# Kernel tuning notes

Measured on AMD Instinct MI355X. Metric: run time of the kernel, lower is better.

Reference implementation:

```python
import jax, jax.numpy as jnp
import numpy as np

HIDDEN = 1024
HEADS = 16
D_K = HIDDEN // HEADS
NEG_INF = -jnp.inf


def setup_inputs() -> dict:
    key = jax.random.key(0)
    ks = jax.random.split(key, 9)
    N, S = 4, 2048
    scale = 1.0 / np.sqrt(HIDDEN)
    x = jax.random.normal(ks[0], (N, S, HIDDEN), dtype=jnp.float32)
    attn_mask = jnp.ones((N, S), dtype=jnp.int32)
    Wq = jax.random.normal(ks[1], (HIDDEN, HIDDEN), dtype=jnp.float32) * scale
    bq = jnp.zeros((HIDDEN,), dtype=jnp.float32)
    Wk = jax.random.normal(ks[2], (HIDDEN, HIDDEN), dtype=jnp.float32) * scale
    bk = jnp.zeros((HIDDEN,), dtype=jnp.float32)
    Wv = jax.random.normal(ks[3], (HIDDEN, HIDDEN), dtype=jnp.float32) * scale
    bv = jnp.zeros((HIDDEN,), dtype=jnp.float32)
    Wp = jax.random.normal(ks[4], (HIDDEN, HIDDEN), dtype=jnp.float32) * scale
    bp = jnp.zeros((HIDDEN,), dtype=jnp.float32)
    return {"x": x, "attn_mask": attn_mask, "Wq": Wq, "bq": bq,
            "Wk": Wk, "bk": bk, "Wv": Wv, "bv": bv, "Wp": Wp, "bp": bp}


def reference(x, attn_mask, Wq, bq, Wk, bk, Wv, bv, Wp, bp):
    N, S, _ = x.shape
    H, dk = HEADS, D_K
    # torch nn.Linear: y = x @ W.T + b
    q = (x @ Wq.T + bq).reshape(N, S, H, dk).transpose(0, 2, 1, 3)  # (N,H,S,dk)
    k = (x @ Wk.T + bk).reshape(N, S, H, dk).transpose(0, 2, 1, 3)
    v = (x @ Wv.T + bv).reshape(N, S, H, dk).transpose(0, 2, 1, 3)
    attn = jnp.einsum('nhqd,nhkd->nhqk', q, k) / jnp.sqrt(jnp.float32(dk))
    mask = attn_mask.reshape(N, 1, 1, S)
    attn = jnp.where(mask == 0, NEG_INF, attn)
    attn = jax.nn.softmax(attn, axis=-1)
    # dropout is identity in eval mode
    y = jnp.einsum('nhqk,nhkd->nhqd', attn, v)  # (N,H,S,dk)
    y = y.transpose(0, 2, 1, 3).reshape(N, S, H * dk)
    return y @ Wp.T + bp
```

## Files before the change

kernel.cpp:

```cpp
#include <hip/hip_runtime.h>

typedef unsigned short u16;
typedef unsigned int u32;
typedef unsigned long long u64;
typedef __attribute__((ext_vector_type(8))) short bf16x8;
typedef __attribute__((ext_vector_type(4))) short bf16x4;
typedef __attribute__((ext_vector_type(4))) float f32x4;
typedef __attribute__((ext_vector_type(2))) unsigned int u32x2;

#define AS1(p) ((const __attribute__((address_space(1))) void*)(p))
#define AS3(p) ((__attribute__((address_space(3))) void*)(p))

__device__ __forceinline__ u16 f2bf(float f) {
    u32 u = __float_as_uint(f);
    u += 0x7fff + ((u >> 16) & 1);
    return (u16)(u >> 16);
}
__device__ __forceinline__ u32 pack2bf(float lo, float hi) {
    u32 a = __float_as_uint(lo) + 0x8000u;
    u32 b = __float_as_uint(hi) + 0x8000u;
    return __builtin_amdgcn_perm(b, a, 0x07060302);
}
__device__ __forceinline__ u32 cvtpk(float lo, float hi) {
    u32 r;
    asm("v_cvt_pk_bf16_f32 %0, %1, %2" : "=v"(r) : "v"(lo), "v"(hi));
    return r;
}

__device__ __forceinline__ void async16(const u16* g, u16* l) {
    __builtin_amdgcn_global_load_lds(AS1(g), AS3(l), 16, 0, 0);
}

__global__ __launch_bounds__(256) void cvt_kernel(const float* __restrict__ src,
                                                  u16* __restrict__ dst, int n) {
    int idx = (blockIdx.x * 256 + threadIdx.x) * 8;
    if (idx >= n) return;
    float4 a = *(const float4*)(src + idx);
    float4 b = *(const float4*)(src + idx + 4);
    uint4 o;
    o.x = (u32)f2bf(a.x) | ((u32)f2bf(a.y) << 16);
    o.y = (u32)f2bf(a.z) | ((u32)f2bf(a.w) << 16);
    o.z = (u32)f2bf(b.x) | ((u32)f2bf(b.y) << 16);
    o.w = (u32)f2bf(b.z) | ((u32)f2bf(b.w) << 16);
    *(uint4*)(dst + idx) = o;
}

__global__ __launch_bounds__(256) void cvt4_kernel(
    const float* __restrict__ s0, const float* __restrict__ s1,
    const float* __restrict__ s2, const float* __restrict__ s3,
    u16* __restrict__ d0, u16* __restrict__ d1,
    u16* __restrict__ d2, u16* __restrict__ d3) {
    const float* s; u16* d;
    switch (blockIdx.y) {
        case 0:  s = s0; d = d0; break;
        case 1:  s = s1; d = d1; break;
        case 2:  s = s2; d = d2; break;
        default: s = s3; d = d3; break;
    }
    int idx = (blockIdx.x * 256 + threadIdx.x) * 8;
    float4 a = *(const float4*)(s + idx);
    float4 b = *(const float4*)(s + idx + 4);
    uint4 o;
    o.x = (u32)f2bf(a.x) | ((u32)f2bf(a.y) << 16);
    o.y = (u32)f2bf(a.z) | ((u32)f2bf(a.w) << 16);
    o.z = (u32)f2bf(b.x) | ((u32)f2bf(b.y) << 16);
    o.w = (u32)f2bf(b.z) | ((u32)f2bf(b.w) << 16);
    *(uint4*)(d + idx) = o;
}

__global__ __launch_bounds__(256, 2) void gemm_bt(
    const u16* __restrict__ A,
    const u16* __restrict__ Wa, const u16* __restrict__ Wb, const u16* __restrict__ Wc,
    const float* __restrict__ ba, const float* __restrict__ bb, const float* __restrict__ bc,
    void* oa, void* ob_, void* oc, int mode)
{
    constexpr int K = 1024;
    __shared__ u16 smem[128 * 132];
    u16* At = smem;
    u16* Wt = smem + 4096;

    const int tid = threadIdx.x;
    const int lane = tid & 63, wv = tid >> 6;
    const int l15 = lane & 15, quad = lane >> 4;
    const int wr = wv >> 1, wc = wv & 1;

    const int L = blockIdx.x + (blockIdx.y << 3) + (blockIdx.z << 9);
    const int g = L & 7;
    const int j = L >> 3;
    const int z = j >> 6;
    const int r = j & 63;
    const int m0 = ((g << 3) + (r & 7)) * 128;
    const int n0 = (r >> 3) * 128;

    const u16* W = (z == 0) ? Wa : ((z == 1) ? Wb : Wc);
    const float* bs = (z == 0) ? ba : ((z == 1) ? bb : bc);
    void* out = (z == 0) ? oa : ((z == 1) ? ob_ : oc);
    const bool swap_ = (mode == 1) || (z < 2);

    f32x4 acc[4][4];
#pragma unroll
    for (int i = 0; i < 4; ++i)
#pragma unroll
        for (int j2 = 0; j2 < 4; ++j2) acc[i][j2] = (f32x4)0.f;

    const int call0 = wv * 2;
    for (int kk = 0; kk < K; kk += 32) {
#pragma unroll
        for (int jj = 0; jj < 2; ++jj) {
            int c = (call0 + jj) * 64 + lane;
            int row = c >> 2;
            int ko = ((c & 3) ^ (row & 3)) * 8;
            async16(A + (size_t)(m0 + row) * K + kk + ko, &At[(call0 + jj) * 512 + lane * 8]);
            async16(W + (size_t)(n0 + row) * K + kk + ko, &Wt[(call0 + jj) * 512 + lane * 8]);
        }
        __syncthreads();

        bf16x8 af[4], wf[4];
#pragma unroll
        for (int t = 0; t < 4; ++t) {
            int rowa = wr * 64 + t * 16 + l15;
            af[t] = *(const bf16x8*)&At[rowa * 32 + ((quad ^ (rowa & 3)) * 8)];
            int rowb = wc * 64 + t * 16 + l15;
            wf[t] = *(const bf16x8*)&Wt[rowb * 32 + ((quad ^ (rowb & 3)) * 8)];
        }
        if (swap_) {
#pragma unroll
            for (int rt = 0; rt < 4; ++rt)
#pragma unroll
                for (int ct = 0; ct < 4; ++ct)
                    acc[rt][ct] = __builtin_amdgcn_mfma_f32_16x16x32_bf16(wf[ct], af[rt], acc[rt][ct], 0, 0, 0);
        } else {
#pragma unroll
            for (int rt = 0; rt < 4; ++rt)
#pragma unroll
                for (int ct = 0; ct < 4; ++ct)
                    acc[rt][ct] = __builtin_amdgcn_mfma_f32_16x16x32_bf16(af[rt], wf[ct], acc[rt][ct], 0, 0, 0);
        }
        __syncthreads();
    }

    if (mode == 1) {
#pragma unroll
        for (int rt = 0; rt < 4; ++rt)
#pragma unroll
            for (int ct = 0; ct < 4; ++ct) {
                int m_ = m0 + wr * 64 + rt * 16 + l15;
                int ob = n0 + wc * 64 + ct * 16 + quad * 4;
                float4 b4 = *(const float4*)&bs[ob];
                float4 v;
                v.x = acc[rt][ct][0] + b4.x;
                v.y = acc[rt][ct][1] + b4.y;
                v.z = acc[rt][ct][2] + b4.z;
                v.w = acc[rt][ct][3] + b4.w;
                *(float4*)((float*)out + (size_t)m_ * 1024 + ob) = v;
            }
        return;
    }

    const int n = m0 >> 11, s0 = m0 & 2047;
    if (z < 2) {
        const float qs = (z == 0) ? 0.18033688011112042f : 1.0f;
#pragma unroll
        for (int rt = 0; rt < 4; ++rt)
#pragma unroll
            for (int ct = 0; ct < 4; ++ct) {
                int ml = wr * 64 + rt * 16 + l15;
                int ol = wc * 64 + ct * 16 + quad * 4;
                float4 b4 = *(const float4*)&bs[n0 + ol];
                float v0 = (acc[rt][ct][0] + b4.x) * qs;
                float v1 = (acc[rt][ct][1] + b4.y) * qs;
                float v2 = (acc[rt][ct][2] + b4.z) * qs;
                float v3 = (acc[rt][ct][3] + b4.w) * qs;
                u32x2 pv = { pack2bf(v0, v1), pack2bf(v2, v3) };
                *(u32x2*)&smem[ml * 132 + ol] = pv;
            }
        __syncthreads();
        const int h0 = n0 >> 6;
#pragma unroll
        for (int p = 0; p < 8; ++p) {
            int hh = p >> 2, qq = p & 3;
            int m = qq * 32 + (tid >> 3), d = (tid & 7) * 8;
            bf16x8 vv = *(const bf16x8*)&smem[m * 132 + hh * 64 + d];
            u16* dst = (u16*)out + ((size_t)((n * 16 + h0 + hh) * 2048 + s0 + m)) * 64 + d;
            *(bf16x8*)dst = vv;
        }
    } else {
#pragma unroll
        for (int rt = 0; rt < 4; ++rt)
#pragma unroll
            for (int ct = 0; ct < 4; ++ct) {
                int ol = wc * 64 + ct * 16 + l15;
                int ml = wr * 64 + rt * 16 + quad * 4;
                float b = bs[n0 + ol];
                float v0 = acc[rt][ct][0] + b;
                float v1 = acc[rt][ct][1] + b;
                float v2 = acc[rt][ct][2] + b;
                float v3 = acc[rt][ct][3] + b;
                u32x2 pv = { pack2bf(v0, v1), pack2bf(v2, v3) };
                *(u32x2*)&smem[ol * 132 + ml] = pv;
            }
        __syncthreads();
#pragma unroll
        for (int p = 0; p < 8; ++p) {
            int o = p * 16 + (tid >> 4), ms = (tid & 15) * 8;
            bf16x8 vv = *(const bf16x8*)&smem[o * 132 + ms];
            int og = n0 + o;
            int h = og >> 6, d = og & 63;
            u16* dst = (u16*)out + ((size_t)((n * 16 + h) * 64 + d)) * 2048 + s0 + ms;
            *(bf16x8*)dst = vv;
        }
    }
}

__global__ __launch_bounds__(256) void attn_kernel(
    const u16* __restrict__ Q, const u16* __restrict__ K_,
    const u16* __restrict__ VT, const int* __restrict__ mask,
    u16* __restrict__ Y)
{
    constexpr int S = 2048, DK = 64, STR = 72;
    __shared__ u16 Kt[2][64 * STR];
    __shared__ u16 Vt[2][64 * STR];
    __shared__ int mtile[2][64];

    const int tid = threadIdx.x;
    const int lane = tid & 63, w = tid >> 6;
    const int l15 = lane & 15, quad = lane >> 4;

    const int L = blockIdx.x + (blockIdx.y << 4);
    const int vb = (L & 7) * 128 + (L >> 3);
    const int nh = vb >> 4;
    const int n = nh >> 4, h = nh & 15;
    const int qbase = (vb & 15) * 128;

    const u16* Qh = Q + (size_t)nh * S * DK;
    const u16* Kh = K_ + (size_t)nh * S * DK;
    const u16* Vh = VT + (size_t)nh * DK * S;

    bf16x8 qf[2][2];
#pragma unroll
    for (int nt = 0; nt < 2; ++nt)
#pragma unroll
        for (int st = 0; st < 2; ++st)
            qf[nt][st] = *(const bf16x8*)(Qh + (size_t)(qbase + w * 32 + nt * 16 + l15) * DK + st * 32 + quad * 8);

    f32x4 o[4][2];
#pragma unroll
    for (int dt = 0; dt < 4; ++dt)
#pragma unroll
        for (int nt = 0; nt < 2; ++nt) o[dt][nt] = (f32x4)0.f;
    float lsum[2] = {0.f, 0.f};

    const int r0 = tid >> 3, c8 = (tid & 7) * 8;

    {
        bf16x8 k0 = *(const bf16x8*)(Kh + (size_t)r0 * 64 + c8);
        bf16x8 k1 = *(const bf16x8*)(Kh + (size_t)(r0 + 32) * 64 + c8);
        bf16x8 v0 = *(const bf16x8*)(Vh + (size_t)r0 * S + c8);
        bf16x8 v1 = *(const bf16x8*)(Vh + (size_t)(r0 + 32) * S + c8);
        *(bf16x8*)&Kt[0][r0 * STR + c8] = k0;
        *(bf16x8*)&Kt[0][(r0 + 32) * STR + c8] = k1;
        *(bf16x8*)&Vt[0][r0 * STR + c8] = v0;
        *(bf16x8*)&Vt[0][(r0 + 32) * STR + c8] = v1;
        if (tid < 64) mtile[0][tid] = mask[n * S + tid];
    }
    __syncthreads();

    const f32x4 zf = (f32x4)0.f;

    for (int it = 0; it < 32; ++it) {
        const int cur = it & 1, nxt = cur ^ 1;
        const u16* Ktc = &Kt[cur][0];
        const u16* Vtc = &Vt[cur][0];

        const int kkn = ((it + 1) << 6) & (S - 1);
        bf16x8 rk0 = *(const bf16x8*)(Kh + (size_t)(kkn + r0) * 64 + c8);
        bf16x8 rk1 = *(const bf16x8*)(Kh + (size_t)(kkn + r0 + 32) * 64 + c8);
        bf16x8 rv0 = *(const bf16x8*)(Vh + (size_t)r0 * S + kkn + c8);
        bf16x8 rv1 = *(const bf16x8*)(Vh + (size_t)(r0 + 32) * S + kkn + c8);
        int mreg = 0;
        if (tid < 64) mreg = mask[n * S + kkn + tid];

        f32x4 sacc[4][2];
        __builtin_amdgcn_s_setprio(1);
#pragma unroll
        for (int jt = 0; jt < 4; ++jt) {
            bf16x8 kf = *(const bf16x8*)&Ktc[(jt * 16 + l15) * STR + quad * 8];
            sacc[jt][0] = __builtin_amdgcn_mfma_f32_16x16x32_bf16(kf, qf[0][0], zf, 0, 0, 0);
            sacc[jt][1] = __builtin_amdgcn_mfma_f32_16x16x32_bf16(kf, qf[1][0], zf, 0, 0, 0);
        }
#pragma unroll
        for (int jt = 0; jt < 4; ++jt) {
            bf16x8 kf = *(const bf16x8*)&Ktc[(jt * 16 + l15) * STR + 32 + quad * 8];
            sacc[jt][0] = __builtin_amdgcn_mfma_f32_16x16x32_bf16(kf, qf[0][1], sacc[jt][0], 0, 0, 0);
            sacc[jt][1] = __builtin_amdgcn_mfma_f32_16x16x32_bf16(kf, qf[1][1], sacc[jt][1], 0, 0, 0);
        }
        __builtin_amdgcn_s_setprio(0);

        const bool fast = (__ballot(mtile[cur][lane] != 0) == ~0ull);
        if (!fast) {
#pragma unroll
            for (int jt = 0; jt < 4; ++jt)
#pragma unroll
                for (int r = 0; r < 4; ++r) {
                    int mv = mtile[cur][jt * 16 + quad * 4 + r];
#pragma unroll
                    for (int nt = 0; nt < 2; ++nt)
                        if (mv == 0) sacc[jt][nt][r] = -1e30f;
                }
        }

        bf16x8 pb[2][2];
#pragma unroll
        for (int nt = 0; nt < 2; ++nt) {
            float ps = 0.f;
            u32 pkx[4], pky[4];
#pragma unroll
            for (int jt = 0; jt < 4; ++jt) {
                float e0 = __builtin_amdgcn_exp2f(sacc[jt][nt][0]);
                float e1 = __builtin_amdgcn_exp2f(sacc[jt][nt][1]);
                float e2 = __builtin_amdgcn_exp2f(sacc[jt][nt][2]);
                float e3 = __builtin_amdgcn_exp2f(sacc[jt][nt][3]);
                ps += (e0 + e1) + (e2 + e3);
                pkx[jt] = cvtpk(e0, e1);
                pky[jt] = cvtpk(e2, e3);
            }
            lsum[nt] += ps;
#pragma unroll
            for (int kt = 0; kt < 2; ++kt) {
                auto rX = __builtin_amdgcn_permlane32_swap(pkx[2 * kt], pkx[2 * kt + 1], false, false);
                auto rY = __builtin_amdgcn_permlane32_swap(pky[2 * kt], pky[2 * kt + 1], false, false);
                auto sX = __builtin_amdgcn_permlane16_swap(rX[0], rX[1], false, false);
                auto sY = __builtin_amdgcn_permlane16_swap(rY[0], rY[1], false, false);
                union { u32 u[4]; bf16x8 v; } pu;
                pu.u[0] = sX[0];
                pu.u[1] = sY[0];
                pu.u[2] = sX[1];
                pu.u[3] = sY[1];
                pb[nt][kt] = pu.v;
            }
        }

        *(bf16x8*)&Kt[nxt][r0 * STR + c8] = rk0;
        *(bf16x8*)&Kt[nxt][(r0 + 32) * STR + c8] = rk1;
        *(bf16x8*)&Vt[nxt][r0 * STR + c8] = rv0;
        *(bf16x8*)&Vt[nxt][(r0 + 32) * STR + c8] = rv1;
        if (tid < 64) mtile[nxt][tid] = mreg;

        __builtin_amdgcn_s_setprio(1);
#pragma unroll
        for (int kt = 0; kt < 2; ++kt) {
#pragma unroll
            for (int dt = 0; dt < 4; ++dt) {
                bf16x8 vf = *(const bf16x8*)&Vtc[(dt * 16 + l15) * STR + kt * 32 + quad * 8];
                o[dt][0] = __builtin_amdgcn_mfma_f32_16x16x32_bf16(vf, pb[0][kt], o[dt][0], 0, 0, 0);
                o[dt][1] = __builtin_amdgcn_mfma_f32_16x16x32_bf16(vf, pb[1][kt], o[dt][1], 0, 0, 0);
            }
        }
        __builtin_amdgcn_s_setprio(0);

        __syncthreads();
    }

#pragma unroll
    for (int nt = 0; nt < 2; ++nt) {
        float ls = lsum[nt];
        ls += __shfl_xor(ls, 16);
        ls += __shfl_xor(ls, 32);
        float rl = (ls > 0.f) ? 1.f / ls : 0.f;
        int qi = qbase + w * 32 + nt * 16 + l15;
#pragma unroll
        for (int dt = 0; dt < 4; ++dt) {
            u32x2 pv = { pack2bf(o[dt][nt][0] * rl, o[dt][nt][1] * rl),
                         pack2bf(o[dt][nt][2] * rl, o[dt][nt][3] * rl) };
            size_t base = ((size_t)(n * 2048 + qi)) * 1024 + h * 64 + dt * 16 + quad * 4;
            *(u32x2*)(Y + base) = pv;
        }
    }
}

extern "C" void kernel_launch(void* const* d_in, const int* in_sizes, int n_in,
                              void* d_out, int out_size, void* d_ws, size_t ws_size,
                              hipStream_t stream) {
    const float* x  = (const float*)d_in[0];
    const int* mask = (const int*)d_in[1];
    const float* Wq = (const float*)d_in[2];
    const float* bq = (const float*)d_in[3];
    const float* Wk = (const float*)d_in[4];
    const float* bk = (const float*)d_in[5];
    const float* Wv = (const float*)d_in[6];
    const float* bv = (const float*)d_in[7];
    const float* Wp = (const float*)d_in[8];
    const float* bp = (const float*)d_in[9];

    char* ws = (char*)d_ws;
    u16* xb  = (u16*)(ws);
    u16* wqb = (u16*)(ws + (16u << 20));
    u16* wkb = (u16*)(ws + (18u << 20));
    u16* wvb = (u16*)(ws + (20u << 20));
    u16* wpb = (u16*)(ws + (22u << 20));
    u16* Qb  = (u16*)(ws + (24u << 20));
    u16* Kb  = (u16*)(ws + (40u << 20));
    u16* Vb  = (u16*)(ws + (56u << 20));
    u16* Yb  = (u16*)(ws + (72u << 20));

    cvt_kernel<<<4096, 256, 0, stream>>>(x, xb, 8388608);
    cvt4_kernel<<<dim3(512, 4), 256, 0, stream>>>(Wq, Wk, Wv, Wp, wqb, wkb, wvb, wpb);

    gemm_bt<<<dim3(8, 64, 3), 256, 0, stream>>>(xb, wqb, wkb, wvb, bq, bk, bv,
                                                (void*)Qb, (void*)Kb, (void*)Vb, 0);

    attn_kernel<<<dim3(16, 64), 256, 0, stream>>>(Qb, Kb, Vb, mask, Yb);

    gemm_bt<<<dim3(8, 64, 1), 256, 0, stream>>>(Yb, wpb, wpb, wpb, bp, bp, bp,
                                                d_out, d_out, d_out, 1);
}
```

Baseline: 303.8 us.

## Double query rows per attention block and precompute mask bitmap upfront

Each attention block now handles 256 query rows (64 per wave) instead of 128, so every K/V tile staged in shared memory is reused by twice as many MFMAs and K/V global traffic is halved. The grid shrinks to 512 blocks and launch bounds request 2 blocks per SM. The per-tile mask staging in shared memory is replaced by a 32-bit all-ones bitmap computed before the loop, with a fallback that reads the mask from global memory. The cost is higher register pressure from larger accumulator and score arrays, fewer blocks in flight, and a serial upfront mask scan.

New measurement: 277.1 us. -8.8%, faster.

```diff
diff --git a/kernel.cpp b/kernel.cpp
--- a/kernel.cpp
+++ b/kernel.cpp
@@ -212,7 +212,7 @@
     }
 }
 
-__global__ __launch_bounds__(256) void attn_kernel(
+__global__ __launch_bounds__(256, 2) void attn_kernel(
     const u16* __restrict__ Q, const u16* __restrict__ K_,
     const u16* __restrict__ VT, const int* __restrict__ mask,
     u16* __restrict__ Y)
@@ -220,37 +220,42 @@
     constexpr int S = 2048, DK = 64, STR = 72;
     __shared__ u16 Kt[2][64 * STR];
     __shared__ u16 Vt[2][64 * STR];
-    __shared__ int mtile[2][64];
 
     const int tid = threadIdx.x;
     const int lane = tid & 63, w = tid >> 6;
     const int l15 = lane & 15, quad = lane >> 4;
 
-    const int L = blockIdx.x + (blockIdx.y << 4);
-    const int vb = (L & 7) * 128 + (L >> 3);
-    const int nh = vb >> 4;
+    const int L = blockIdx.x + (blockIdx.y << 3);
+    const int vb = (L & 7) * 64 + (L >> 3);
+    const int nh = vb >> 3;
     const int n = nh >> 4, h = nh & 15;
-    const int qbase = (vb & 15) * 128;
+    const int qbase = (vb & 7) * 256;
 
     const u16* Qh = Q + (size_t)nh * S * DK;
     const u16* Kh = K_ + (size_t)nh * S * DK;
     const u16* Vh = VT + (size_t)nh * DK * S;
 
-    bf16x8 qf[2][2];
-#pragma unroll
-    for (int nt = 0; nt < 2; ++nt)
+    bf16x8 qf[4][2];
+#pragma unroll
+    for (int nt = 0; nt < 4; ++nt)
 #pragma unroll
         for (int st = 0; st < 2; ++st)
-            qf[nt][st] = *(const bf16x8*)(Qh + (size_t)(qbase + w * 32 + nt * 16 + l15) * DK + st * 32 + quad * 8);
-
-    f32x4 o[4][2];
+            qf[nt][st] = *(const bf16x8*)(Qh + (size_t)(qbase + w * 64 + nt * 16 + l15) * DK + st * 32 + quad * 8);
+
+    f32x4 o[4][4];
 #pragma unroll
     for (int dt = 0; dt < 4; ++dt)
 #pragma unroll
-        for (int nt = 0; nt < 2; ++nt) o[dt][nt] = (f32x4)0.f;
-    float lsum[2] = {0.f, 0.f};
+        for (int nt = 0; nt < 4; ++nt) o[dt][nt] = (f32x4)0.f;
+    float lsum[4] = {0.f, 0.f, 0.f, 0.f};
 
     const int r0 = tid >> 3, c8 = (tid & 7) * 8;
+
+    u32 bm = 0;
+    for (int t = 0; t < 32; ++t) {
+        int mv = mask[n * S + t * 64 + lane];
+        if (__ballot(mv != 0) == ~0ull) bm |= (1u << t);
+    }
 
     {
         bf16x8 k0 = *(const bf16x8*)(Kh + (size_t)r0 * 64 + c8);
@@ -261,7 +266,6 @@
         *(bf16x8*)&Kt[0][(r0 + 32) * STR + c8] = k1;
         *(bf16x8*)&Vt[0][r0 * STR + c8] = v0;
         *(bf16x8*)&Vt[0][(r0 + 32) * STR + c8] = v1;
-        if (tid < 64) mtile[0][tid] = mask[n * S + tid];
     }
     __syncthreads();
 
@@ -277,41 +281,40 @@
         bf16x8 rk1 = *(const bf16x8*)(Kh + (size_t)(kkn + r0 + 32) * 64 + c8);
         bf16x8 rv0 = *(const bf16x8*)(Vh + (size_t)r0 * S + kkn + c8);
         bf16x8 rv1 = *(const bf16x8*)(Vh + (size_t)(r0 + 32) * S + kkn + c8);
-        int mreg = 0;
-        if (tid < 64) mreg = mask[n * S + kkn + tid];
-
-        f32x4 sacc[4][2];
+
+        f32x4 sacc[4][4];
         __builtin_amdgcn_s_setprio(1);
 #pragma unroll
         for (int jt = 0; jt < 4; ++jt) {
             bf16x8 kf = *(const bf16x8*)&Ktc[(jt * 16 + l15) * STR + quad * 8];
-            sacc[jt][0] = __builtin_amdgcn_mfma_f32_16x16x32_bf16(kf, qf[0][0], zf, 0, 0, 0);
-            sacc[jt][1] = __builtin_amdgcn_mfma_f32_16x16x32_bf16(kf, qf[1][0], zf, 0, 0, 0);
+#pragma unroll
+            for (int nt = 0; nt < 4; ++nt)
+                sacc[jt][nt] = __builtin_amdgcn_mfma_f32_16x16x32_bf16(kf, qf[nt][0], zf, 0, 0, 0);
         }
 #pragma unroll
         for (int jt = 0; jt < 4; ++jt) {
             bf16x8 kf = *(const bf16x8*)&Ktc[(jt * 16 + l15) * STR + 32 + quad * 8];
-            sacc[jt][0] = __builtin_amdgcn_mfma_f32_16x16x32_bf16(kf, qf[0][1], sacc[jt][0], 0, 0, 0);
-            sacc[jt][1] = __builtin_amdgcn_mfma_f32_16x16x32_bf16(kf, qf[1][1], sacc[jt][1], 0, 0, 0);
+#pragma unroll
+            for (int nt = 0; nt < 4; ++nt)
+                sacc[jt][nt] = __builtin_amdgcn_mfma_f32_16x16x32_bf16(kf, qf[nt][1], sacc[jt][nt], 0, 0, 0);
         }
         __builtin_amdgcn_s_setprio(0);
 
-        const bool fast = (__ballot(mtile[cur][lane] != 0) == ~0ull);
-        if (!fast) {
+        if (!((bm >> it) & 1)) {
 #pragma unroll
             for (int jt = 0; jt < 4; ++jt)
 #pragma unroll
                 for (int r = 0; r < 4; ++r) {
-                    int mv = mtile[cur][jt * 16 + quad * 4 + r];
-#pragma unroll
-                    for (int nt = 0; nt < 2; ++nt)
+                    int mv = mask[n * S + it * 64 + jt * 16 + quad * 4 + r];
+#pragma unroll
+                    for (int nt = 0; nt < 4; ++nt)
                         if (mv == 0) sacc[jt][nt][r] = -1e30f;
                 }
         }
 
-        bf16x8 pb[2][2];
-#pragma unroll
-        for (int nt = 0; nt < 2; ++nt) {
+        bf16x8 pb[4][2];
+#pragma unroll
+        for (int nt = 0; nt < 4; ++nt) {
             float ps = 0.f;
             u32 pkx[4], pky[4];
 #pragma unroll
@@ -344,7 +347,6 @@
         *(bf16x8*)&Kt[nxt][(r0 + 32) * STR + c8] = rk1;
         *(bf16x8*)&Vt[nxt][r0 * STR + c8] = rv0;
         *(bf16x8*)&Vt[nxt][(r0 + 32) * STR + c8] = rv1;
-        if (tid < 64) mtile[nxt][tid] = mreg;
 
         __builtin_amdgcn_s_setprio(1);
 #pragma unroll
@@ -352,8 +354,9 @@
 #pragma unroll
             for (int dt = 0; dt < 4; ++dt) {
                 bf16x8 vf = *(const bf16x8*)&Vtc[(dt * 16 + l15) * STR + kt * 32 + quad * 8];
-                o[dt][0] = __builtin_amdgcn_mfma_f32_16x16x32_bf16(vf, pb[0][kt], o[dt][0], 0, 0, 0);
-                o[dt][1] = __builtin_amdgcn_mfma_f32_16x16x32_bf16(vf, pb[1][kt], o[dt][1], 0, 0, 0);
+#pragma unroll
+                for (int nt = 0; nt < 4; ++nt)
+                    o[dt][nt] = __builtin_amdgcn_mfma_f32_16x16x32_bf16(vf, pb[nt][kt], o[dt][nt], 0, 0, 0);
             }
         }
         __builtin_amdgcn_s_setprio(0);
@@ -362,12 +365,12 @@
     }
 
 #pragma unroll
-    for (int nt = 0; nt < 2; ++nt) {
+    for (int nt = 0; nt < 4; ++nt) {
         float ls = lsum[nt];
         ls += __shfl_xor(ls, 16);
         ls += __shfl_xor(ls, 32);
         float rl = (ls > 0.f) ? 1.f / ls : 0.f;
-        int qi = qbase + w * 32 + nt * 16 + l15;
+        int qi = qbase + w * 64 + nt * 16 + l15;
 #pragma unroll
         for (int dt = 0; dt < 4; ++dt) {
             u32x2 pv = { pack2bf(o[dt][nt][0] * rl, o[dt][nt][1] * rl),
@@ -409,7 +412,7 @@
     gemm_bt<<<dim3(8, 64, 3), 256, 0, stream>>>(xb, wqb, wkb, wvb, bq, bk, bv,
                                                 (void*)Qb, (void*)Kb, (void*)Vb, 0);
 
-    attn_kernel<<<dim3(16, 64), 256, 0, stream>>>(Qb, Kb, Vb, mask, Yb);
+    attn_kernel<<<dim3(8, 64), 256, 0, stream>>>(Qb, Kb, Vb, mask, Yb);
 
     gemm_bt<<<dim3(8, 64, 1), 256, 0, stream>>>(Yb, wpb, wpb, wpb, bp, bp, bp,
                                                 d_out, d_out, d_out, 1);
```
